# Optimization experiments

Hardware: AMD Instinct MI355X
Metric: run time of the kernel (lower is better)

Reference implementation:

```python
import jax, jax.numpy as jnp
import numpy as np

N = 100_000   # nodes
E = 1_600_000 # edges
F = 128       # feature_dim
H = 128       # hidden_dim
C = 16        # num_classes


def setup_inputs() -> dict:
    key = jax.random.key(0)
    ks = jax.random.split(key, 7)
    x = jax.random.normal(ks[0], (N, F), dtype=jnp.float32)
    edge_index = jax.random.randint(ks[1], (2, E), 0, N, dtype=jnp.int64)
    edge_attr = jax.random.uniform(ks[2], (E,), dtype=jnp.float32)
    W1 = jax.random.normal(ks[3], (F, H), dtype=jnp.float32) / np.float32(np.sqrt(F))
    b1 = jnp.zeros((H,), jnp.float32)
    W2 = jax.random.normal(ks[4], (H, C), dtype=jnp.float32) / np.float32(np.sqrt(H))
    b2 = jnp.zeros((C,), jnp.float32)
    return {"x": x, "edge_index": edge_index, "edge_attr": edge_attr,
            "W1": W1, "b1": b1, "W2": W2, "b2": b2}


def gcn_conv(x, src, dst, ew, W, b, n):
    # PyG GCNConv: add self-loops (weight 1), symmetric degree normalization,
    # linear transform, weighted scatter-sum to destinations, bias after aggregation.
    loop = jnp.arange(n, dtype=src.dtype)
    s = jnp.concatenate([src, loop])
    d = jnp.concatenate([dst, loop])
    w = jnp.concatenate([ew, jnp.ones((n,), ew.dtype)])
    deg = jax.ops.segment_sum(w, d, num_segments=n)           # [N]
    dinv = jnp.where(deg > 0, jax.lax.rsqrt(deg), 0.0)
    norm = dinv[s] * w * dinv[d]                               # [E+N]
    h = x @ W                                                  # [N, out]
    out = jax.ops.segment_sum(h[s] * norm[:, None], d, num_segments=n)
    return out + b


def reference(x, edge_index, edge_attr, W1, b1, W2, b2):
    src, dst = edge_index[0], edge_index[1]
    h = gcn_conv(x, src, dst, edge_attr, W1, b1, N)
    h = jax.nn.relu(h)
    # dropout is identity in eval mode
    h = gcn_conv(h, src, dst, edge_attr, W2, b2, N)
    return jax.nn.softmax(h, axis=1)
```

## Files before the change

kernel.cpp:

```cpp
#include <hip/hip_runtime.h>
#include <hip/hip_fp16.h>
#include <math.h>

#define SCAN_CHUNK 2048
#define NBLK 256
#define BSH 9
#define BNODES 512


typedef __attribute__((ext_vector_type(8))) _Float16 f16x8;
typedef __attribute__((ext_vector_type(16))) float f32x16;


__global__ __launch_bounds__(256) void k_prep(const float* __restrict__ W,
                                              __half* __restrict__ W1f) {
    int tid = blockIdx.x * 256 + threadIdx.x;
    if (tid < 16384) {
        int j  = tid & 7;
        int l  = (tid >> 3) & 63;
        int ks = (tid >> 9) & 7;
        int cb = tid >> 12;
        int c = cb * 32 + (l & 31);
        int k = (l >> 5) * 8 + ks * 16 + j;
        W1f[tid] = __float2half(W[(size_t)k * 128 + c]);
    }
}


__device__ __forceinline__ void gemm1_mfma(const float* __restrict__ x,
                                           const __half* __restrict__ W1f,
                                           __half* __restrict__ h1, int n,
                                           int row0, int t, char* smem) {
    __half (*xs)[136] = (__half (*)[136])smem;
#pragma unroll
    for (int it = 0; it < 4; ++it) {
        int idx = it * 256 + t;
        int r = idx >> 5, c4 = (idx & 31) * 4;
        int gr = row0 + r;
        float4 v = (gr < n) ? *(const float4*)(x + (size_t)gr * 128 + c4)
                            : make_float4(0.f, 0.f, 0.f, 0.f);
        union { __half2 h[2]; uint2 u; } pk;
        pk.h[0] = __floats2half2_rn(v.x, v.y);
        pk.h[1] = __floats2half2_rn(v.z, v.w);
        *(uint2*)&xs[r][c4] = pk.u;
    }
    __syncthreads();

    int wv = t >> 6, lane = t & 63;
    int m = lane & 31, kh = lane >> 5;
    int col0 = wv * 32;

    f16x8 a[8], b[8];
    const __half* bp = W1f + ((size_t)wv * 8 * 64 + lane) * 8;
#pragma unroll
    for (int ks = 0; ks < 8; ++ks)
        b[ks] = *(const f16x8*)(bp + (size_t)ks * 64 * 8);
#pragma unroll
    for (int ks = 0; ks < 8; ++ks)
        a[ks] = *(const f16x8*)&xs[m][kh * 8 + ks * 16];

    f32x16 acc;
#pragma unroll
    for (int r = 0; r < 16; ++r) acc[r] = 0.f;
#pragma unroll
    for (int ks = 0; ks < 8; ++ks)
        acc = __builtin_amdgcn_mfma_f32_32x32x16_f16(a[ks], b[ks], acc, 0, 0, 0);

#pragma unroll
    for (int r = 0; r < 16; ++r) {
        int row = (r & 3) + 8 * (r >> 2) + 4 * kh;
        int g = row0 + row;
        if (g < n) h1[(size_t)g * 128 + col0 + m] = __float2half(acc[r]);
    }
}

__device__ __forceinline__ long long sl_begin(int eb, int e) {
    return ((long long)eb * e / NBLK) & ~3LL;
}


__global__ __launch_bounds__(256) void kA(const int* __restrict__ dst, int e,
                                          int* __restrict__ hist, int nbuck,
                                          const float* __restrict__ x,
                                          const __half* __restrict__ W1f,
                                          __half* __restrict__ h1, int n,
                                          int nbB, int nbG, int gbase) {
    __shared__ char smem[32 * 136 * 2];
    int bid = blockIdx.x;
    long long T = nbB + nbG;
    long long g = ((long long)bid * nbG) / T;
    bool is_g = (((long long)(bid + 1) * nbG) / T) > g;
    int t = threadIdx.x;

    if (!is_g) {
        int* cnt = (int*)smem;
        int eb = bid - (int)g;
        for (int j = t; j < nbuck; j += 256) cnt[j] = 0;
        __syncthreads();
        long long e0 = sl_begin(eb, e);
        long long e1 = (eb == NBLK - 1) ? e : sl_begin(eb + 1, e);
        for (long long i = e0 + (long long)t * 4; i + 3 < e1; i += 1024) {
            int4 d4 = *(const int4*)(dst + i);
            atomicAdd(&cnt[d4.x >> BSH], 1);
            atomicAdd(&cnt[d4.y >> BSH], 1);
            atomicAdd(&cnt[d4.z >> BSH], 1);
            atomicAdd(&cnt[d4.w >> BSH], 1);
        }
        long long vend = e0 + ((e1 - e0) & ~3LL);
        for (long long i = vend + t; i < e1; i += 256)
            atomicAdd(&cnt[dst[i] >> BSH], 1);
        __syncthreads();
        for (int j = t; j < nbuck; j += 256)
            hist[(size_t)j * NBLK + eb] = cnt[j];
        return;
    }

    gemm1_mfma(x, W1f, h1, n, (gbase + (int)g) * 32, t, smem);
}


__global__ __launch_bounds__(256) void k_scanh(int* __restrict__ hist,
                                               int* __restrict__ bsum, int nh) {
    __shared__ int sh[256];
    int b = blockIdx.x, t = threadIdx.x;
    int base = b * SCAN_CHUNK + t * 8;
    int v[8];
    int s = 0;
#pragma unroll
    for (int j = 0; j < 8; ++j) {
        int i = base + j;
        v[j] = (i < nh) ? hist[i] : 0;
        s += v[j];
    }
    sh[t] = s;
    __syncthreads();
    for (int off = 1; off < 256; off <<= 1) {
        int u = (t >= off) ? sh[t - off] : 0;
        __syncthreads();
        sh[t] += u;
        __syncthreads();
    }
    int excl = (t > 0) ? sh[t - 1] : 0;
    if (t == 255) bsum[b] = sh[255];
    int run = excl;
#pragma unroll
    for (int j = 0; j < 8; ++j) {
        int i = base + j;
        if (i < nh) hist[i] = run;
        run += v[j];
    }
}

__device__ __forceinline__ void scan_bsum(const int* __restrict__ bsum, int nbS,
                                          int* boffs, int t) {
    if (t < 32) {
        int raw = (t < nbS) ? bsum[t] : 0;
        int v = raw;
        for (int off = 1; off < 32; off <<= 1) {
            int u = __shfl_up(v, off, 64);
            if (t >= off) v += u;
        }
        boffs[t] = v - raw;
    }
}


__global__ __launch_bounds__(256) void kB(const int* __restrict__ src,
                                          const int* __restrict__ dst,
                                          const float* __restrict__ ew, int e,
                                          const int* __restrict__ hist,
                                          const int* __restrict__ bsum, int nbS,
                                          int nbuck,
                                          int2* __restrict__ bucketed,
                                          const float* __restrict__ x,
                                          const __half* __restrict__ W1f,
                                          __half* __restrict__ h1, int n,
                                          int nbB, int nbG, int gbase) {
    __shared__ char smem[32 * 136 * 2];
    int bid = blockIdx.x;
    long long T = nbB + nbG;
    long long g = ((long long)bid * nbG) / T;
    bool is_g = (((long long)(bid + 1) * nbG) / T) > g;
    int t = threadIdx.x;

    if (!is_g) {
        int* wc = (int*)smem;
        int* boffs = (int*)(smem + 2048);
        int eb = bid - (int)g;
        scan_bsum(bsum, nbS, boffs, t);
        __syncthreads();
        for (int j = t; j < nbuck; j += 256) {
            int idx = j * NBLK + eb;
            wc[j] = hist[idx] + boffs[idx >> 11];
        }
        __syncthreads();
        long long e0 = sl_begin(eb, e);
        long long e1 = (eb == NBLK - 1) ? e : sl_begin(eb + 1, e);
        for (long long i = e0 + (long long)t * 4; i + 3 < e1; i += 1024) {
            int4 d4 = *(const int4*)(dst + i);
            int4 s4 = *(const int4*)(src + i);
            float4 w4 = *(const float4*)(ew + i);
            int2 rec;
            int pos;
            pos = atomicAdd(&wc[d4.x >> BSH], 1);
            rec.x = s4.x | ((d4.x & (BNODES - 1)) << 17);
            rec.y = __float_as_int(w4.x);
            bucketed[pos] = rec;
            pos = atomicAdd(&wc[d4.y >> BSH], 1);
            rec.x = s4.y | ((d4.y & (BNODES - 1)) << 17);
            rec.y = __float_as_int(w4.y);
            bucketed[pos] = rec;
            pos = atomicAdd(&wc[d4.z >> BSH], 1);
            rec.x = s4.z | ((d4.z & (BNODES - 1)) << 17);
            rec.y = __float_as_int(w4.z);
            bucketed[pos] = rec;
            pos = atomicAdd(&wc[d4.w >> BSH], 1);
            rec.x = s4.w | ((d4.w & (BNODES - 1)) << 17);
            rec.y = __float_as_int(w4.w);
            bucketed[pos] = rec;
        }
        long long vend = e0 + ((e1 - e0) & ~3LL);
        for (long long i = vend + t; i < e1; i += 256) {
            int d = dst[i];
            int b = d >> BSH;
            int pos = atomicAdd(&wc[b], 1);
            int2 rec;
            rec.x = src[i] | ((d & (BNODES - 1)) << 17);
            rec.y = __float_as_int(ew[i]);
            bucketed[pos] = rec;
        }
        return;
    }

    gemm1_mfma(x, W1f, h1, n, (gbase + (int)g) * 32, t, smem);
}


__global__ __launch_bounds__(256) void kC1(const int2* __restrict__ bucketed,
                                           const int* __restrict__ hist,
                                           const int* __restrict__ bsum, int nbS,
                                           int nbuck, int n, int e,
                                           int2* __restrict__ nodeinfo,
                                           const float* __restrict__ x,
                                           const __half* __restrict__ W1f,
                                           __half* __restrict__ h1, int gbase) {
    __shared__ char smem[32 * 136 * 2];
    int bid = blockIdx.x, t = threadIdx.x;

    if (bid >= nbuck) {
        gemm1_mfma(x, W1f, h1, n, (gbase + bid - nbuck) * 32, t, smem);
        return;
    }

    unsigned long long* cd = (unsigned long long*)smem;
    int* sh    = (int*)(smem + 4096);
    int* boffs = (int*)(smem + 5120);
    int b = bid;

    scan_bsum(bsum, nbS, boffs, t);
    cd[t] = 0ULL; cd[t + 256] = 0ULL;
    __syncthreads();

    int i0 = b * NBLK;
    int bstart = hist[i0] + boffs[i0 >> 11];
    int bend;
    if (b == nbuck - 1) bend = e;
    else {
        int i1 = (b + 1) * NBLK;
        bend = hist[i1] + boffs[i1 >> 11];
    }

    for (int i = bstart + t; i < bend; i += 256) {
        int2 rec = bucketed[i];
        int l = (rec.x >> 17) & (BNODES - 1);
        unsigned long long pk = (1ULL << 52) |
            (unsigned long long)(long long)rintf(__int_as_float(rec.y) * 67108864.0f);
        atomicAdd(&cd[l], pk);
    }
    __syncthreads();

    unsigned long long v0 = cd[2 * t], v1 = cd[2 * t + 1];
    int c0 = (int)(v0 >> 52), c1 = (int)(v1 >> 52);
    float d0 = (float)(long long)(v0 & ((1ULL << 52) - 1)) * 1.4901161193847656e-8f;
    float d1 = (float)(long long)(v1 & ((1ULL << 52) - 1)) * 1.4901161193847656e-8f;
    sh[t] = c0 + c1;
    __syncthreads();
    for (int off = 1; off < 256; off <<= 1) {
        int u = (t >= off) ? sh[t - off] : 0;
        __syncthreads();
        sh[t] += u;
        __syncthreads();
    }
    int excl = (t > 0) ? sh[t - 1] : 0;

    int rs0 = bstart + excl;
    int rs1 = rs0 + c0;
#pragma unroll
    for (int q = 0; q < 2; ++q) {
        int l = 2 * t + q;
        float dv = 1.0f / sqrtf(1.0f + ((q == 0) ? d0 : d1));
        int gnode = b * BNODES + l;
        if (gnode < n) {
            int2 ni;
            ni.x = (q == 0) ? rs0 : rs1;
            ni.y = __float_as_int(dv);
            nodeinfo[gnode] = ni;
        }
    }
    if (b == nbuck - 1 && t == 0) {
        int2 sent; sent.x = e; sent.y = 0;
        nodeinfo[n] = sent;
    }
}


__global__ __launch_bounds__(256) void kC2(const int2* __restrict__ bucketed,
                                           const int* __restrict__ hist,
                                           const int* __restrict__ bsum, int nbS,
                                           int nbuck, int n, int e,
                                           int2* __restrict__ csr,
                                           const int2* __restrict__ nodeinfo,
                                           const float* __restrict__ x,
                                           const __half* __restrict__ W1f,
                                           __half* __restrict__ h1, int gbase) {
    __shared__ char smem[32 * 136 * 2];
    int bid = blockIdx.x, t = threadIdx.x;

    if (bid >= nbuck) {
        gemm1_mfma(x, W1f, h1, n, (gbase + bid - nbuck) * 32, t, smem);
        return;
    }

    int* wcs   = (int*)smem;
    int* boffs = (int*)(smem + 2048);
    int b = bid;
    const int* nis = (const int*)nodeinfo;

    scan_bsum(bsum, nbS, boffs, t);
#pragma unroll
    for (int q = 0; q < 2; ++q) {
        int l = t + q * 256;
        int gnode = b * BNODES + l;
        wcs[l] = (gnode < n) ? nis[2 * (size_t)gnode] : 0;
    }
    __syncthreads();

    int i0 = b * NBLK;
    int bstart = hist[i0] + boffs[i0 >> 11];
    int bend;
    if (b == nbuck - 1) bend = e;
    else {
        int i1 = (b + 1) * NBLK;
        bend = hist[i1] + boffs[i1 >> 11];
    }

    for (int i = bstart + t; i < bend; i += 256) {
        int2 rec = bucketed[i];
        int l = (rec.x >> 17) & (BNODES - 1);
        int s = rec.x & 0x1FFFF;
        float dv = __int_as_float(nis[2 * (size_t)s + 1]);
        int pos = atomicAdd(&wcs[l], 1);
        int2 o;
        o.x = s;
        o.y = __float_as_int(__int_as_float(rec.y) * dv);
        csr[pos] = o;
    }
}


__global__ __launch_bounds__(256) void k_agg1(const __half* __restrict__ h1,
                                              const int2* __restrict__ nodeinfo,
                                              const int2* __restrict__ csr,
                                              const float* __restrict__ b1,
                                              const float* __restrict__ W2g,
                                              __half* __restrict__ h2, int n) {
    __shared__ float a1s[4][128];
    __shared__ float wt[16][132];
    int t = threadIdx.x;
#pragma unroll
    for (int it = 0; it < 8; ++it) {
        int idx = it * 256 + t;
        wt[idx & 15][idx >> 4] = W2g[idx];
    }
    int wv = t >> 6;
    int lane = t & 63;
    int grp = lane >> 4;
    int sl = lane & 15;
    int i = blockIdx.x * 4 + wv;
    float acc[8];
#pragma unroll
    for (int k = 0; k < 8; ++k) acc[k] = 0.f;
    float di = 0.f;
    if (i < n) {
        int2 ni = nodeinfo[i];
        int begin = ni.x;
        int end = ((const int*)nodeinfo)[(size_t)(i + 1) * 2];
        di = __int_as_float(ni.y);
        if (grp == 0) {
            uint4 sv = *((const uint4*)(h1 + (size_t)i * 128) + sl);
            const __half2* hp = (const __half2*)&sv;
#pragma unroll
            for (int k = 0; k < 4; ++k) {
                float2 f = __half22float2(hp[k]);
                acc[2 * k] = di * f.x; acc[2 * k + 1] = di * f.y;
            }
        }
        int len = end - begin;
        int m = (len + 3) >> 2;
        if (m > 0) {
            int j0 = begin + grp;
            bool v0 = j0 < end;
            int2 er0 = csr[v0 ? j0 : begin];
            float w0 = v0 ? __int_as_float(er0.y) : 0.f;
            uint4 hv0 = *((const uint4*)(h1 + (size_t)er0.x * 128) + sl);
            int j1 = j0 + 4;
            bool v1 = j1 < end;
            int2 er1 = csr[v1 ? j1 : begin];
            float w1 = v1 ? __int_as_float(er1.y) : 0.f;
            for (int it2 = 1; it2 < m; ++it2) {
                uint4 hv1 = *((const uint4*)(h1 + (size_t)er1.x * 128) + sl);
                int j2 = j1 + 4;
                bool v2 = j2 < end;
                int2 er2 = csr[v2 ? j2 : begin];
                float w2 = v2 ? __int_as_float(er2.y) : 0.f;
                const __half2* hp = (const __half2*)&hv0;
#pragma unroll
                for (int k = 0; k < 4; ++k) {
                    float2 f = __half22float2(hp[k]);
                    acc[2 * k]     += w0 * f.x;
                    acc[2 * k + 1] += w0 * f.y;
                }
                hv0 = hv1; w0 = w1;
                er1 = er2; w1 = w2; j1 = j2;
            }
            const __half2* hp = (const __half2*)&hv0;
#pragma unroll
            for (int k = 0; k < 4; ++k) {
                float2 f = __half22float2(hp[k]);
                acc[2 * k]     += w0 * f.x;
                acc[2 * k + 1] += w0 * f.y;
            }
        }
    }
#pragma unroll
    for (int k = 0; k < 8; ++k) {
        acc[k] += __shfl_xor(acc[k], 16, 64);
        acc[k] += __shfl_xor(acc[k], 32, 64);
    }
    if (i < n && grp == 0) {
#pragma unroll
        for (int k = 0; k < 8; ++k)
            a1s[wv][8 * sl + k] = fmaxf(di * acc[k] + b1[8 * sl + k], 0.f);
    }
    __syncthreads();
    int oi = t >> 2, q = t & 3;
    int node = oi >> 4, c = oi & 15;
    const float* arow = a1s[node];
    float accd = 0.f;
#pragma unroll
    for (int j = 0; j < 32; ++j) accd += arow[q + 4 * j] * wt[c][q + 4 * j];
    accd += __shfl_xor(accd, 1, 64);
    accd += __shfl_xor(accd, 2, 64);
    int gi = blockIdx.x * 4 + node;
    if (q == 0 && gi < n) h2[(size_t)gi * 16 + c] = __float2half(accd);
}


__global__ __launch_bounds__(256) void k_agg2(const __half* __restrict__ h2,
                                              const int2* __restrict__ nodeinfo,
                                              const int2* __restrict__ csr,
                                              const float* __restrict__ b2,
                                              float* __restrict__ out, int n) {
    int t = blockIdx.x * 256 + threadIdx.x;
    int i = t >> 3;
    int cp = t & 7;
    if (i >= n) return;
    int2 ni = nodeinfo[i];
    int begin = ni.x;
    int end = ((const int*)nodeinfo)[(size_t)(i + 1) * 2];
    float di = __int_as_float(ni.y);
    const __half2* h2p = (const __half2*)h2;
    float2 self = __half22float2(h2p[(size_t)i * 8 + cp]);
    float a0 = di * self.x, a1 = di * self.y;
    int j = begin;
    for (; j + 4 <= end; j += 4) {
        int2 e0 = csr[j], e1 = csr[j + 1], e2 = csr[j + 2], e3 = csr[j + 3];
        float2 f0 = __half22float2(h2p[(size_t)e0.x * 8 + cp]);
        float2 f1 = __half22float2(h2p[(size_t)e1.x * 8 + cp]);
        float2 f2 = __half22float2(h2p[(size_t)e2.x * 8 + cp]);
        float2 f3 = __half22float2(h2p[(size_t)e3.x * 8 + cp]);
        float w0 = __int_as_float(e0.y), w1 = __int_as_float(e1.y);
        float w2 = __int_as_float(e2.y), w3 = __int_as_float(e3.y);
        a0 += w0 * f0.x; a1 += w0 * f0.y;
        a0 += w1 * f1.x; a1 += w1 * f1.y;
        a0 += w2 * f2.x; a1 += w2 * f2.y;
        a0 += w3 * f3.x; a1 += w3 * f3.y;
    }
    for (; j < end; ++j) {
        int2 e0 = csr[j];
        float2 f0 = __half22float2(h2p[(size_t)e0.x * 8 + cp]);
        float w0 = __int_as_float(e0.y);
        a0 += w0 * f0.x; a1 += w0 * f0.y;
    }
    float2 bb = *(const float2*)(b2 + 2 * cp);
    a0 = di * a0 + bb.x;
    a1 = di * a1 + bb.y;
    float m = fmaxf(a0, a1);
    for (int off = 4; off; off >>= 1) m = fmaxf(m, __shfl_xor(m, off, 8));
    float ex0 = expf(a0 - m), ex1 = expf(a1 - m);
    float s = ex0 + ex1;
    for (int off = 4; off; off >>= 1) s += __shfl_xor(s, off, 8);
    float2 o; o.x = ex0 / s; o.y = ex1 / s;
    *(float2*)(out + (size_t)i * 16 + 2 * cp) = o;
}


extern "C" void kernel_launch(void* const* d_in, const int* in_sizes, int n_in,
                              void* d_out, int out_size, void* d_ws, size_t ws_size,
                              hipStream_t stream) {
    const float* x  = (const float*)d_in[0];
    const int*   ei = (const int*)d_in[1];
    const float* ew = (const float*)d_in[2];
    const float* W1 = (const float*)d_in[3];
    const float* b1 = (const float*)d_in[4];
    const float* W2 = (const float*)d_in[5];
    const float* b2 = (const float*)d_in[6];
    float* out = (float*)d_out;

    const int N = in_sizes[0] / 128;
    const int E = in_sizes[2];
    const int* src = ei;
    const int* dst = ei + E;

    const int nbuck = (N + BNODES - 1) >> BSH;
    const int nh = nbuck * NBLK;
    const int nbS = (nh + SCAN_CHUNK - 1) / SCAN_CHUNK;

    char* w = (char*)d_ws;
    int2*   bucketed = (int2*)w;              w += (size_t)E * 8;
    int2*   csr      = (int2*)w;              w += (size_t)E * 8;
    __half* h1       = (__half*)w;            w += (size_t)N * 128 * 2;
    __half* h2       = (__half*)w;            w += (size_t)N * 16 * 2;
    int2*   nodeinfo = (int2*)w;              w += (size_t)(N + 2) * 8;
    int*    hist     = (int*)w;               w += (size_t)nh * 4;
    int*    bsum     = (int*)w;               w += 64 * 4;
    __half* W1f      = (__half*)w;            w += (size_t)16384 * 2;

    int nbG_total = (N + 31) / 32;
    int nbG1 = 1450;
    int nbG2 = 1150;
    int nbG3 = 275;
    int nbG4 = nbG_total - nbG1 - nbG2 - nbG3;

    k_prep<<<64, 256, 0, stream>>>(W1, W1f);
    kA<<<NBLK + nbG1, 256, 0, stream>>>(dst, E, hist, nbuck, x, W1f, h1, N,
                                        NBLK, nbG1, 0);
    k_scanh<<<nbS, 256, 0, stream>>>(hist, bsum, nh);
    kB<<<NBLK + nbG2, 256, 0, stream>>>(src, dst, ew, E, hist, bsum, nbS, nbuck,
                                        bucketed, x, W1f, h1, N, NBLK, nbG2, nbG1);
    kC1<<<nbuck + nbG3, 256, 0, stream>>>(bucketed, hist, bsum, nbS, nbuck, N, E,
                                          nodeinfo, x, W1f, h1, nbG1 + nbG2);
    kC2<<<nbuck + nbG4, 256, 0, stream>>>(bucketed, hist, bsum, nbS, nbuck, N, E,
                                          csr, nodeinfo, x, W1f, h1,
                                          nbG1 + nbG2 + nbG3);
    k_agg1<<<(N + 3) / 4, 256, 0, stream>>>(h1, nodeinfo, csr, b1, W2, h2, N);
    k_agg2<<<(N + 31) / 32, 256, 0, stream>>>(h2, nodeinfo, csr, b2, out, N);
}
```

Measured before the change: 178.7 us.

## Process four GEMM row tiles per block with double-buffered LDS prefetch

```diff
diff --git a/kernel.cpp b/kernel.cpp
--- a/kernel.cpp
+++ b/kernel.cpp
@@ -6,10 +6,13 @@
 #define NBLK 256
 #define BSH 9
 #define BNODES 512
+#define NT 4
 
 
 typedef __attribute__((ext_vector_type(8))) _Float16 f16x8;
 typedef __attribute__((ext_vector_type(16))) float f32x16;
+
+#define GEMM_SMEM (64 * 136 * 2)
 
 
 __global__ __launch_bounds__(256) void k_prep(const float* __restrict__ W,
@@ -27,50 +30,87 @@
 }
 
 
-__device__ __forceinline__ void gemm1_mfma(const float* __restrict__ x,
-                                           const __half* __restrict__ W1f,
-                                           __half* __restrict__ h1, int n,
-                                           int row0, int t, char* smem) {
+__device__ __forceinline__ void gemm1_tiles(const float* __restrict__ x,
+                                            const __half* __restrict__ W1f,
+                                            __half* __restrict__ h1, int n,
+                                            int tile0, int t, char* smem) {
     __half (*xs)[136] = (__half (*)[136])smem;
-#pragma unroll
-    for (int it = 0; it < 4; ++it) {
-        int idx = it * 256 + t;
-        int r = idx >> 5, c4 = (idx & 31) * 4;
-        int gr = row0 + r;
-        float4 v = (gr < n) ? *(const float4*)(x + (size_t)gr * 128 + c4)
-                            : make_float4(0.f, 0.f, 0.f, 0.f);
-        union { __half2 h[2]; uint2 u; } pk;
-        pk.h[0] = __floats2half2_rn(v.x, v.y);
-        pk.h[1] = __floats2half2_rn(v.z, v.w);
-        *(uint2*)&xs[r][c4] = pk.u;
-    }
-    __syncthreads();
+    int ntt = (n + 31) >> 5;
+    int ntile = ntt - tile0;
+    if (ntile > NT) ntile = NT;
 
     int wv = t >> 6, lane = t & 63;
     int m = lane & 31, kh = lane >> 5;
     int col0 = wv * 32;
 
-    f16x8 a[8], b[8];
+    f16x8 b[8];
     const __half* bp = W1f + ((size_t)wv * 8 * 64 + lane) * 8;
 #pragma unroll
     for (int ks = 0; ks < 8; ++ks)
         b[ks] = *(const f16x8*)(bp + (size_t)ks * 64 * 8);
-#pragma unroll
-    for (int ks = 0; ks < 8; ++ks)
-        a[ks] = *(const f16x8*)&xs[m][kh * 8 + ks * 16];
-
-    f32x16 acc;
-#pragma unroll
-    for (int r = 0; r < 16; ++r) acc[r] = 0.f;
-#pragma unroll
-    for (int ks = 0; ks < 8; ++ks)
-        acc = __builtin_amdgcn_mfma_f32_32x32x16_f16(a[ks], b[ks], acc, 0, 0, 0);
-
-#pragma unroll
-    for (int r = 0; r < 16; ++r) {
-        int row = (r & 3) + 8 * (r >> 2) + 4 * kh;
-        int g = row0 + row;
-        if (g < n) h1[(size_t)g * 128 + col0 + m] = __float2half(acc[r]);
+
+    float4 v[4];
+    int row0 = tile0 * 32;
+#pragma unroll
+    for (int it = 0; it < 4; ++it) {
+        int idx = it * 256 + t;
+        int rr = idx >> 5, c4 = (idx & 31) * 4;
+        int gr = row0 + rr;
+        v[it] = (gr < n) ? *(const float4*)(x + (size_t)gr * 128 + c4)
+                         : make_float4(0.f, 0.f, 0.f, 0.f);
+    }
+    int cur = 0;
+#pragma unroll
+    for (int it = 0; it < 4; ++it) {
+        int idx = it * 256 + t;
+        int rr = idx >> 5, c4 = (idx & 31) * 4;
+        union { __half2 h[2]; uint2 u; } pk;
+        pk.h[0] = __floats2half2_rn(v[it].x, v[it].y);
+        pk.h[1] = __floats2half2_rn(v[it].z, v[it].w);
+        *(uint2*)&xs[rr][c4] = pk.u;
+    }
+    __syncthreads();
+
+    for (int tt = 0; tt < ntile; ++tt) {
+        int rowc = (tile0 + tt) * 32;
+        if (tt + 1 < ntile) {
+            int rown = rowc + 32;
+#pragma unroll
+            for (int it = 0; it < 4; ++it) {
+                int idx = it * 256 + t;
+                int rr = idx >> 5, c4 = (idx & 31) * 4;
+                int gr = rown + rr;
+                v[it] = (gr < n) ? *(const float4*)(x + (size_t)gr * 128 + c4)
+                                 : make_float4(0.f, 0.f, 0.f, 0.f);
+            }
+        }
+        f32x16 acc;
+#pragma unroll
+        for (int q = 0; q < 16; ++q) acc[q] = 0.f;
+#pragma unroll
+        for (int ks = 0; ks < 8; ++ks) {
+            f16x8 a = *(const f16x8*)&xs[cur * 32 + m][kh * 8 + ks * 16];
+            acc = __builtin_amdgcn_mfma_f32_32x32x16_f16(a, b[ks], acc, 0, 0, 0);
+        }
+#pragma unroll
+        for (int q = 0; q < 16; ++q) {
+            int row = (q & 3) + 8 * (q >> 2) + 4 * kh;
+            int g = rowc + row;
+            if (g < n) h1[(size_t)g * 128 + col0 + m] = __float2half(acc[q]);
+        }
+        if (tt + 1 < ntile) {
+#pragma unroll
+            for (int it = 0; it < 4; ++it) {
+                int idx = it * 256 + t;
+                int rr = idx >> 5, c4 = (idx & 31) * 4;
+                union { __half2 h[2]; uint2 u; } pk;
+                pk.h[0] = __floats2half2_rn(v[it].x, v[it].y);
+                pk.h[1] = __floats2half2_rn(v[it].z, v[it].w);
+                *(uint2*)&xs[(cur ^ 1) * 32 + rr][c4] = pk.u;
+            }
+            __syncthreads();
+            cur ^= 1;
+        }
     }
 }
 
@@ -85,7 +125,7 @@
                                           const __half* __restrict__ W1f,
                                           __half* __restrict__ h1, int n,
                                           int nbB, int nbG, int gbase) {
-    __shared__ char smem[32 * 136 * 2];
+    __shared__ char smem[GEMM_SMEM];
     int bid = blockIdx.x;
     long long T = nbB + nbG;
     long long g = ((long long)bid * nbG) / T;
@@ -115,7 +155,7 @@
         return;
     }
 
-    gemm1_mfma(x, W1f, h1, n, (gbase + (int)g) * 32, t, smem);
+    gemm1_tiles(x, W1f, h1, n, (gbase + (int)g) * NT, t, smem);
 }
 
 
@@ -176,7 +216,7 @@
                                           const __half* __restrict__ W1f,
                                           __half* __restrict__ h1, int n,
                                           int nbB, int nbG, int gbase) {
-    __shared__ char smem[32 * 136 * 2];
+    __shared__ char smem[GEMM_SMEM];
     int bid = blockIdx.x;
     long long T = nbB + nbG;
     long long g = ((long long)bid * nbG) / T;
@@ -232,7 +272,7 @@
         return;
     }
 
-    gemm1_mfma(x, W1f, h1, n, (gbase + (int)g) * 32, t, smem);
+    gemm1_tiles(x, W1f, h1, n, (gbase + (int)g) * NT, t, smem);
 }
 
 
@@ -244,11 +284,11 @@
                                            const float* __restrict__ x,
                                            const __half* __restrict__ W1f,
                                            __half* __restrict__ h1, int gbase) {
-    __shared__ char smem[32 * 136 * 2];
+    __shared__ char smem[GEMM_SMEM];
     int bid = blockIdx.x, t = threadIdx.x;
 
     if (bid >= nbuck) {
-        gemm1_mfma(x, W1f, h1, n, (gbase + bid - nbuck) * 32, t, smem);
+        gemm1_tiles(x, W1f, h1, n, (gbase + bid - nbuck) * NT, t, smem);
         return;
     }
 
@@ -323,11 +363,11 @@
                                            const float* __restrict__ x,
                                            const __half* __restrict__ W1f,
                                            __half* __restrict__ h1, int gbase) {
-    __shared__ char smem[32 * 136 * 2];
+    __shared__ char smem[GEMM_SMEM];
     int bid = blockIdx.x, t = threadIdx.x;
 
     if (bid >= nbuck) {
-        gemm1_mfma(x, W1f, h1, n, (gbase + bid - nbuck) * 32, t, smem);
+        gemm1_tiles(x, W1f, h1, n, (gbase + bid - nbuck) * NT, t, smem);
         return;
     }
 
@@ -546,23 +586,24 @@
     int*    bsum     = (int*)w;               w += 64 * 4;
     __half* W1f      = (__half*)w;            w += (size_t)16384 * 2;
 
-    int nbG_total = (N + 31) / 32;
-    int nbG1 = 1450;
-    int nbG2 = 1150;
-    int nbG3 = 275;
-    int nbG4 = nbG_total - nbG1 - nbG2 - nbG3;
+    int ntiles = (N + 31) / 32;
+    int tbTotal = (ntiles + NT - 1) / NT;
+    int tbA = 360;
+    int tbB = 290;
+    int tbC1 = 70;
+    int tbC2 = tbTotal - tbA - tbB - tbC1;
 
     k_prep<<<64, 256, 0, stream>>>(W1, W1f);
-    kA<<<NBLK + nbG1, 256, 0, stream>>>(dst, E, hist, nbuck, x, W1f, h1, N,
-                                        NBLK, nbG1, 0);
+    kA<<<NBLK + tbA, 256, 0, stream>>>(dst, E, hist, nbuck, x, W1f, h1, N,
+                                       NBLK, tbA, 0);
     k_scanh<<<nbS, 256, 0, stream>>>(hist, bsum, nh);
-    kB<<<NBLK + nbG2, 256, 0, stream>>>(src, dst, ew, E, hist, bsum, nbS, nbuck,
-                                        bucketed, x, W1f, h1, N, NBLK, nbG2, nbG1);
-    kC1<<<nbuck + nbG3, 256, 0, stream>>>(bucketed, hist, bsum, nbS, nbuck, N, E,
-                                          nodeinfo, x, W1f, h1, nbG1 + nbG2);
-    kC2<<<nbuck + nbG4, 256, 0, stream>>>(bucketed, hist, bsum, nbS, nbuck, N, E,
+    kB<<<NBLK + tbB, 256, 0, stream>>>(src, dst, ew, E, hist, bsum, nbS, nbuck,
+                                       bucketed, x, W1f, h1, N, NBLK, tbB, tbA);
+    kC1<<<nbuck + tbC1, 256, 0, stream>>>(bucketed, hist, bsum, nbS, nbuck, N, E,
+                                          nodeinfo, x, W1f, h1, tbA + tbB);
+    kC2<<<nbuck + tbC2, 256, 0, stream>>>(bucketed, hist, bsum, nbS, nbuck, N, E,
                                           csr, nodeinfo, x, W1f, h1,
-                                          nbG1 + nbG2 + nbG3);
+                                          tbA + tbB + tbC1);
     k_agg1<<<(N + 3) / 4, 256, 0, stream>>>(h1, nodeinfo, csr, b1, W2, h2, N);
     k_agg2<<<(N + 31) / 32, 256, 0, stream>>>(h2, nodeinfo, csr, b2, out, N);
 }
```

Measured after the change: 180.4 us. No clear change (+0.9%).

## Merge CSR build and GEMM1 into one cooperative persistent kernel

Applied to the files above, without the earlier changes.

```diff
diff --git a/kernel.cpp b/kernel.cpp
--- a/kernel.cpp
+++ b/kernel.cpp
@@ -1,11 +1,14 @@
 #include <hip/hip_runtime.h>
 #include <hip/hip_fp16.h>
+#include <hip/hip_cooperative_groups.h>
 #include <math.h>
 
-#define SCAN_CHUNK 2048
+namespace cg = cooperative_groups;
+
 #define NBLK 256
 #define BSH 9
 #define BNODES 512
+#define CG_GRID 512
 
 
 typedef __attribute__((ext_vector_type(8))) _Float16 f16x8;
@@ -13,7 +16,10 @@
 
 
 __global__ __launch_bounds__(256) void k_prep(const float* __restrict__ W,
-                                              __half* __restrict__ W1f) {
+                                              __half* __restrict__ W1f,
+                                              int* __restrict__ tot,
+                                              int* __restrict__ gcur,
+                                              int* __restrict__ ctrs) {
     int tid = blockIdx.x * 256 + threadIdx.x;
     if (tid < 16384) {
         int j  = tid & 7;
@@ -24,14 +30,20 @@
         int k = (l >> 5) * 8 + ks * 16 + j;
         W1f[tid] = __float2half(W[(size_t)k * 128 + c]);
     }
-}
-
-
-__device__ __forceinline__ void gemm1_mfma(const float* __restrict__ x,
-                                           const __half* __restrict__ W1f,
-                                           __half* __restrict__ h1, int n,
-                                           int row0, int t, char* smem) {
+    if (tid < 256) { tot[tid] = 0; gcur[tid] = 0; }
+    if (tid < 8) ctrs[tid] = 0;
+}
+
+__device__ __forceinline__ long long sl_begin(int eb, int e) {
+    return ((long long)eb * e / NBLK) & ~3LL;
+}
+
+__device__ __forceinline__ void do_gemm(const float* __restrict__ x,
+                                        const f16x8 b[8],
+                                        __half* __restrict__ h1, int n,
+                                        int tile, int t, char* smem) {
     __half (*xs)[136] = (__half (*)[136])smem;
+    int row0 = tile * 32;
 #pragma unroll
     for (int it = 0; it < 4; ++it) {
         int idx = it * 256 + t;
@@ -45,58 +57,64 @@
         *(uint2*)&xs[r][c4] = pk.u;
     }
     __syncthreads();
-
     int wv = t >> 6, lane = t & 63;
     int m = lane & 31, kh = lane >> 5;
     int col0 = wv * 32;
-
-    f16x8 a[8], b[8];
-    const __half* bp = W1f + ((size_t)wv * 8 * 64 + lane) * 8;
-#pragma unroll
-    for (int ks = 0; ks < 8; ++ks)
-        b[ks] = *(const f16x8*)(bp + (size_t)ks * 64 * 8);
-#pragma unroll
-    for (int ks = 0; ks < 8; ++ks)
-        a[ks] = *(const f16x8*)&xs[m][kh * 8 + ks * 16];
-
     f32x16 acc;
 #pragma unroll
-    for (int r = 0; r < 16; ++r) acc[r] = 0.f;
-#pragma unroll
-    for (int ks = 0; ks < 8; ++ks)
-        acc = __builtin_amdgcn_mfma_f32_32x32x16_f16(a[ks], b[ks], acc, 0, 0, 0);
-
-#pragma unroll
-    for (int r = 0; r < 16; ++r) {
-        int row = (r & 3) + 8 * (r >> 2) + 4 * kh;
+    for (int q = 0; q < 16; ++q) acc[q] = 0.f;
+#pragma unroll
+    for (int ks = 0; ks < 8; ++ks) {
+        f16x8 a = *(const f16x8*)&xs[m][kh * 8 + ks * 16];
+        acc = __builtin_amdgcn_mfma_f32_32x32x16_f16(a, b[ks], acc, 0, 0, 0);
+    }
+#pragma unroll
+    for (int q = 0; q < 16; ++q) {
+        int row = (q & 3) + 8 * (q >> 2) + 4 * kh;
         int g = row0 + row;
-        if (g < n) h1[(size_t)g * 128 + col0 + m] = __float2half(acc[r]);
-    }
-}
-
-__device__ __forceinline__ long long sl_begin(int eb, int e) {
-    return ((long long)eb * e / NBLK) & ~3LL;
-}
-
-
-__global__ __launch_bounds__(256) void kA(const int* __restrict__ dst, int e,
-                                          int* __restrict__ hist, int nbuck,
-                                          const float* __restrict__ x,
-                                          const __half* __restrict__ W1f,
-                                          __half* __restrict__ h1, int n,
-                                          int nbB, int nbG, int gbase) {
-    __shared__ char smem[32 * 136 * 2];
-    int bid = blockIdx.x;
-    long long T = nbB + nbG;
-    long long g = ((long long)bid * nbG) / T;
-    bool is_g = (((long long)(bid + 1) * nbG) / T) > g;
-    int t = threadIdx.x;
-
-    if (!is_g) {
+        if (g < n) h1[(size_t)g * 128 + col0 + m] = __float2half(acc[q]);
+    }
+}
+
+__device__ __forceinline__ int pull(int* ctr, int lo, int hi, int t, int* sP) {
+    if (t == 0) *sP = lo + atomicAdd(ctr, 1);
+    __syncthreads();
+    int v = *sP;
+    return (v < hi) ? v : -1;
+}
+
+
+__global__ __launch_bounds__(256, 4) void k_coop(
+        const int* __restrict__ src, const int* __restrict__ dst,
+        const float* __restrict__ ew, int e, int nbuck, int n,
+        const float* __restrict__ x, const __half* __restrict__ W1f,
+        __half* __restrict__ h1,
+        int2* __restrict__ bucketed, int2* __restrict__ csr,
+        int2* __restrict__ nodeinfo,
+        int* __restrict__ tot, int* __restrict__ gcur,
+        int* __restrict__ gbase, int* __restrict__ ctrs,
+        int ntiles, int cap1, int cap2, int cap3) {
+    __shared__ char smem[8704];
+    __shared__ int sPull;
+    cg::grid_group grid = cg::this_grid();
+    int bid = blockIdx.x, t = threadIdx.x;
+
+    int wv = t >> 6, lane = t & 63;
+    f16x8 b[8];
+    {
+        const __half* bp = W1f + ((size_t)wv * 8 * 64 + lane) * 8;
+#pragma unroll
+        for (int ks = 0; ks < 8; ++ks)
+            b[ks] = *(const f16x8*)(bp + (size_t)ks * 64 * 8);
+    }
+
+    int c0r = 0, c1r = 0;
+
+    if (bid < NBLK) {
         int* cnt = (int*)smem;
-        int eb = bid - (int)g;
-        for (int j = t; j < nbuck; j += 256) cnt[j] = 0;
-        __syncthreads();
+        cnt[t] = 0; cnt[t + 256] = 0;
+        __syncthreads();
+        int eb = bid;
         long long e0 = sl_begin(eb, e);
         long long e1 = (eb == NBLK - 1) ? e : sl_begin(eb + 1, e);
         for (long long i = e0 + (long long)t * 4; i + 3 < e1; i += 1024) {
@@ -110,90 +128,37 @@
         for (long long i = vend + t; i < e1; i += 256)
             atomicAdd(&cnt[dst[i] >> BSH], 1);
         __syncthreads();
-        for (int j = t; j < nbuck; j += 256)
-            hist[(size_t)j * NBLK + eb] = cnt[j];
-        return;
-    }
-
-    gemm1_mfma(x, W1f, h1, n, (gbase + (int)g) * 32, t, smem);
-}
-
-
-__global__ __launch_bounds__(256) void k_scanh(int* __restrict__ hist,
-                                               int* __restrict__ bsum, int nh) {
-    __shared__ int sh[256];
-    int b = blockIdx.x, t = threadIdx.x;
-    int base = b * SCAN_CHUNK + t * 8;
-    int v[8];
-    int s = 0;
-#pragma unroll
-    for (int j = 0; j < 8; ++j) {
-        int i = base + j;
-        v[j] = (i < nh) ? hist[i] : 0;
-        s += v[j];
-    }
-    sh[t] = s;
-    __syncthreads();
-    for (int off = 1; off < 256; off <<= 1) {
-        int u = (t >= off) ? sh[t - off] : 0;
-        __syncthreads();
-        sh[t] += u;
-        __syncthreads();
-    }
-    int excl = (t > 0) ? sh[t - 1] : 0;
-    if (t == 255) bsum[b] = sh[255];
-    int run = excl;
-#pragma unroll
-    for (int j = 0; j < 8; ++j) {
-        int i = base + j;
-        if (i < nh) hist[i] = run;
-        run += v[j];
-    }
-}
-
-__device__ __forceinline__ void scan_bsum(const int* __restrict__ bsum, int nbS,
-                                          int* boffs, int t) {
-    if (t < 32) {
-        int raw = (t < nbS) ? bsum[t] : 0;
-        int v = raw;
-        for (int off = 1; off < 32; off <<= 1) {
-            int u = __shfl_up(v, off, 64);
-            if (t >= off) v += u;
-        }
-        boffs[t] = v - raw;
-    }
-}
-
-
-__global__ __launch_bounds__(256) void kB(const int* __restrict__ src,
-                                          const int* __restrict__ dst,
-                                          const float* __restrict__ ew, int e,
-                                          const int* __restrict__ hist,
-                                          const int* __restrict__ bsum, int nbS,
-                                          int nbuck,
-                                          int2* __restrict__ bucketed,
-                                          const float* __restrict__ x,
-                                          const __half* __restrict__ W1f,
-                                          __half* __restrict__ h1, int n,
-                                          int nbB, int nbG, int gbase) {
-    __shared__ char smem[32 * 136 * 2];
-    int bid = blockIdx.x;
-    long long T = nbB + nbG;
-    long long g = ((long long)bid * nbG) / T;
-    bool is_g = (((long long)(bid + 1) * nbG) / T) > g;
-    int t = threadIdx.x;
-
-    if (!is_g) {
+        c0r = cnt[2 * t]; c1r = cnt[2 * t + 1];
+        if (2 * t < nbuck && c0r) atomicAdd(&tot[2 * t], c0r);
+        if (2 * t + 1 < nbuck && c1r) atomicAdd(&tot[2 * t + 1], c1r);
+    }
+    for (int tl; (tl = pull(&ctrs[0], 0, cap1, t, &sPull)) >= 0; )
+        do_gemm(x, b, h1, n, tl, t, smem);
+    grid.sync();
+
+    if (bid < NBLK) {
         int* wc = (int*)smem;
-        int* boffs = (int*)(smem + 2048);
-        int eb = bid - (int)g;
-        scan_bsum(bsum, nbS, boffs, t);
-        __syncthreads();
-        for (int j = t; j < nbuck; j += 256) {
-            int idx = j * NBLK + eb;
-            wc[j] = hist[idx] + boffs[idx >> 11];
-        }
-        __syncthreads();
+        int* bb = (int*)(smem + 1024);
+        int tv = (t < nbuck) ? tot[t] : 0;
+        bb[t] = tv;
+        __syncthreads();
+        for (int off = 1; off < 256; off <<= 1) {
+            int u = (t >= off) ? bb[t - off] : 0;
+            __syncthreads();
+            bb[t] += u;
+            __syncthreads();
+        }
+        int ex = bb[t] - tv;
+        if (bid == 0) gbase[t] = ex;
+        __syncthreads();
+        bb[t] = ex;
+        __syncthreads();
+        if (2 * t < nbuck)
+            wc[2 * t] = bb[2 * t] + atomicAdd(&gcur[2 * t], c0r);
+        if (2 * t + 1 < nbuck)
+            wc[2 * t + 1] = bb[2 * t + 1] + atomicAdd(&gcur[2 * t + 1], c1r);
+        __syncthreads();
+        int eb = bid;
         long long e0 = sl_begin(eb, e);
         long long e1 = (eb == NBLK - 1) ? e : sl_begin(eb + 1, e);
         for (long long i = e0 + (long long)t * 4; i + 3 < e1; i += 1024) {
@@ -222,149 +187,94 @@
         long long vend = e0 + ((e1 - e0) & ~3LL);
         for (long long i = vend + t; i < e1; i += 256) {
             int d = dst[i];
-            int b = d >> BSH;
-            int pos = atomicAdd(&wc[b], 1);
+            int pos = atomicAdd(&wc[d >> BSH], 1);
             int2 rec;
             rec.x = src[i] | ((d & (BNODES - 1)) << 17);
             rec.y = __float_as_int(ew[i]);
             bucketed[pos] = rec;
         }
-        return;
-    }
-
-    gemm1_mfma(x, W1f, h1, n, (gbase + (int)g) * 32, t, smem);
-}
-
-
-__global__ __launch_bounds__(256) void kC1(const int2* __restrict__ bucketed,
-                                           const int* __restrict__ hist,
-                                           const int* __restrict__ bsum, int nbS,
-                                           int nbuck, int n, int e,
-                                           int2* __restrict__ nodeinfo,
-                                           const float* __restrict__ x,
-                                           const __half* __restrict__ W1f,
-                                           __half* __restrict__ h1, int gbase) {
-    __shared__ char smem[32 * 136 * 2];
-    int bid = blockIdx.x, t = threadIdx.x;
-
-    if (bid >= nbuck) {
-        gemm1_mfma(x, W1f, h1, n, (gbase + bid - nbuck) * 32, t, smem);
-        return;
-    }
-
-    unsigned long long* cd = (unsigned long long*)smem;
-    int* sh    = (int*)(smem + 4096);
-    int* boffs = (int*)(smem + 5120);
-    int b = bid;
-
-    scan_bsum(bsum, nbS, boffs, t);
-    cd[t] = 0ULL; cd[t + 256] = 0ULL;
-    __syncthreads();
-
-    int i0 = b * NBLK;
-    int bstart = hist[i0] + boffs[i0 >> 11];
-    int bend;
-    if (b == nbuck - 1) bend = e;
-    else {
-        int i1 = (b + 1) * NBLK;
-        bend = hist[i1] + boffs[i1 >> 11];
-    }
-
-    for (int i = bstart + t; i < bend; i += 256) {
-        int2 rec = bucketed[i];
-        int l = (rec.x >> 17) & (BNODES - 1);
-        unsigned long long pk = (1ULL << 52) |
-            (unsigned long long)(long long)rintf(__int_as_float(rec.y) * 67108864.0f);
-        atomicAdd(&cd[l], pk);
-    }
-    __syncthreads();
-
-    unsigned long long v0 = cd[2 * t], v1 = cd[2 * t + 1];
-    int c0 = (int)(v0 >> 52), c1 = (int)(v1 >> 52);
-    float d0 = (float)(long long)(v0 & ((1ULL << 52) - 1)) * 1.4901161193847656e-8f;
-    float d1 = (float)(long long)(v1 & ((1ULL << 52) - 1)) * 1.4901161193847656e-8f;
-    sh[t] = c0 + c1;
-    __syncthreads();
-    for (int off = 1; off < 256; off <<= 1) {
-        int u = (t >= off) ? sh[t - off] : 0;
-        __syncthreads();
-        sh[t] += u;
-        __syncthreads();
-    }
-    int excl = (t > 0) ? sh[t - 1] : 0;
-
-    int rs0 = bstart + excl;
-    int rs1 = rs0 + c0;
-#pragma unroll
-    for (int q = 0; q < 2; ++q) {
-        int l = 2 * t + q;
-        float dv = 1.0f / sqrtf(1.0f + ((q == 0) ? d0 : d1));
-        int gnode = b * BNODES + l;
-        if (gnode < n) {
-            int2 ni;
-            ni.x = (q == 0) ? rs0 : rs1;
-            ni.y = __float_as_int(dv);
-            nodeinfo[gnode] = ni;
-        }
-    }
-    if (b == nbuck - 1 && t == 0) {
-        int2 sent; sent.x = e; sent.y = 0;
-        nodeinfo[n] = sent;
-    }
-}
-
-
-__global__ __launch_bounds__(256) void kC2(const int2* __restrict__ bucketed,
-                                           const int* __restrict__ hist,
-                                           const int* __restrict__ bsum, int nbS,
-                                           int nbuck, int n, int e,
-                                           int2* __restrict__ csr,
-                                           const int2* __restrict__ nodeinfo,
-                                           const float* __restrict__ x,
-                                           const __half* __restrict__ W1f,
-                                           __half* __restrict__ h1, int gbase) {
-    __shared__ char smem[32 * 136 * 2];
-    int bid = blockIdx.x, t = threadIdx.x;
-
-    if (bid >= nbuck) {
-        gemm1_mfma(x, W1f, h1, n, (gbase + bid - nbuck) * 32, t, smem);
-        return;
-    }
-
-    int* wcs   = (int*)smem;
-    int* boffs = (int*)(smem + 2048);
-    int b = bid;
-    const int* nis = (const int*)nodeinfo;
-
-    scan_bsum(bsum, nbS, boffs, t);
-#pragma unroll
-    for (int q = 0; q < 2; ++q) {
-        int l = t + q * 256;
-        int gnode = b * BNODES + l;
-        wcs[l] = (gnode < n) ? nis[2 * (size_t)gnode] : 0;
-    }
-    __syncthreads();
-
-    int i0 = b * NBLK;
-    int bstart = hist[i0] + boffs[i0 >> 11];
-    int bend;
-    if (b == nbuck - 1) bend = e;
-    else {
-        int i1 = (b + 1) * NBLK;
-        bend = hist[i1] + boffs[i1 >> 11];
-    }
-
-    for (int i = bstart + t; i < bend; i += 256) {
-        int2 rec = bucketed[i];
-        int l = (rec.x >> 17) & (BNODES - 1);
-        int s = rec.x & 0x1FFFF;
-        float dv = __int_as_float(nis[2 * (size_t)s + 1]);
-        int pos = atomicAdd(&wcs[l], 1);
-        int2 o;
-        o.x = s;
-        o.y = __float_as_int(__int_as_float(rec.y) * dv);
-        csr[pos] = o;
-    }
+    }
+    for (int tl; (tl = pull(&ctrs[1], cap1, cap2, t, &sPull)) >= 0; )
+        do_gemm(x, b, h1, n, tl, t, smem);
+    grid.sync();
+
+    if (bid < nbuck) {
+        unsigned long long* cd = (unsigned long long*)smem;
+        int* sh = (int*)(smem + 4096);
+        cd[t] = 0ULL; cd[t + 256] = 0ULL;
+        __syncthreads();
+        int bstart = gbase[bid];
+        int bend = (bid == nbuck - 1) ? e : gbase[bid + 1];
+        for (int i = bstart + t; i < bend; i += 256) {
+            int2 rec = bucketed[i];
+            int l = (rec.x >> 17) & (BNODES - 1);
+            unsigned long long pk = (1ULL << 52) |
+                (unsigned long long)(long long)rintf(__int_as_float(rec.y) * 67108864.0f);
+            atomicAdd(&cd[l], pk);
+        }
+        __syncthreads();
+        unsigned long long v0 = cd[2 * t], v1 = cd[2 * t + 1];
+        int cc0 = (int)(v0 >> 52), cc1 = (int)(v1 >> 52);
+        float dd0 = (float)(long long)(v0 & ((1ULL << 52) - 1)) * 1.4901161193847656e-8f;
+        float dd1 = (float)(long long)(v1 & ((1ULL << 52) - 1)) * 1.4901161193847656e-8f;
+        sh[t] = cc0 + cc1;
+        __syncthreads();
+        for (int off = 1; off < 256; off <<= 1) {
+            int u = (t >= off) ? sh[t - off] : 0;
+            __syncthreads();
+            sh[t] += u;
+            __syncthreads();
+        }
+        int excl = (t > 0) ? sh[t - 1] : 0;
+        int rs0 = bstart + excl;
+        int rs1 = rs0 + cc0;
+#pragma unroll
+        for (int q = 0; q < 2; ++q) {
+            int l = 2 * t + q;
+            float dv = 1.0f / sqrtf(1.0f + ((q == 0) ? dd0 : dd1));
+            int gnode = bid * BNODES + l;
+            if (gnode < n) {
+                int2 ni;
+                ni.x = (q == 0) ? rs0 : rs1;
+                ni.y = __float_as_int(dv);
+                nodeinfo[gnode] = ni;
+            }
+        }
+        if (bid == nbuck - 1 && t == 0) {
+            int2 sent; sent.x = e; sent.y = 0;
+            nodeinfo[n] = sent;
+        }
+    }
+    for (int tl; (tl = pull(&ctrs[2], cap2, cap3, t, &sPull)) >= 0; )
+        do_gemm(x, b, h1, n, tl, t, smem);
+    grid.sync();
+
+    if (bid < nbuck) {
+        int* wcs = (int*)smem;
+        const int* nis = (const int*)nodeinfo;
+#pragma unroll
+        for (int q = 0; q < 2; ++q) {
+            int l = t + q * 256;
+            int gnode = bid * BNODES + l;
+            wcs[l] = (gnode < n) ? nis[2 * (size_t)gnode] : 0;
+        }
+        __syncthreads();
+        int bstart = gbase[bid];
+        int bend = (bid == nbuck - 1) ? e : gbase[bid + 1];
+        for (int i = bstart + t; i < bend; i += 256) {
+            int2 rec = bucketed[i];
+            int l = (rec.x >> 17) & (BNODES - 1);
+            int s = rec.x & 0x1FFFF;
+            float dv = __int_as_float(nis[2 * (size_t)s + 1]);
+            int pos = atomicAdd(&wcs[l], 1);
+            int2 o;
+            o.x = s;
+            o.y = __float_as_int(__int_as_float(rec.y) * dv);
+            csr[pos] = o;
+        }
+    }
+    for (int tl; (tl = pull(&ctrs[3], cap3, ntiles, t, &sPull)) >= 0; )
+        do_gemm(x, b, h1, n, tl, t, smem);
 }
 
 
@@ -527,14 +437,12 @@
     const float* b2 = (const float*)d_in[6];
     float* out = (float*)d_out;
 
-    const int N = in_sizes[0] / 128;
-    const int E = in_sizes[2];
+    int N = in_sizes[0] / 128;
+    int E = in_sizes[2];
     const int* src = ei;
     const int* dst = ei + E;
 
-    const int nbuck = (N + BNODES - 1) >> BSH;
-    const int nh = nbuck * NBLK;
-    const int nbS = (nh + SCAN_CHUNK - 1) / SCAN_CHUNK;
+    int nbuck = (N + BNODES - 1) >> BSH;
 
     char* w = (char*)d_ws;
     int2*   bucketed = (int2*)w;              w += (size_t)E * 8;
@@ -542,27 +450,28 @@
     __half* h1       = (__half*)w;            w += (size_t)N * 128 * 2;
     __half* h2       = (__half*)w;            w += (size_t)N * 16 * 2;
     int2*   nodeinfo = (int2*)w;              w += (size_t)(N + 2) * 8;
-    int*    hist     = (int*)w;               w += (size_t)nh * 4;
-    int*    bsum     = (int*)w;               w += 64 * 4;
     __half* W1f      = (__half*)w;            w += (size_t)16384 * 2;
-
-    int nbG_total = (N + 31) / 32;
-    int nbG1 = 1450;
-    int nbG2 = 1150;
-    int nbG3 = 275;
-    int nbG4 = nbG_total - nbG1 - nbG2 - nbG3;
-
-    k_prep<<<64, 256, 0, stream>>>(W1, W1f);
-    kA<<<NBLK + nbG1, 256, 0, stream>>>(dst, E, hist, nbuck, x, W1f, h1, N,
-                                        NBLK, nbG1, 0);
-    k_scanh<<<nbS, 256, 0, stream>>>(hist, bsum, nh);
-    kB<<<NBLK + nbG2, 256, 0, stream>>>(src, dst, ew, E, hist, bsum, nbS, nbuck,
-                                        bucketed, x, W1f, h1, N, NBLK, nbG2, nbG1);
-    kC1<<<nbuck + nbG3, 256, 0, stream>>>(bucketed, hist, bsum, nbS, nbuck, N, E,
-                                          nodeinfo, x, W1f, h1, nbG1 + nbG2);
-    kC2<<<nbuck + nbG4, 256, 0, stream>>>(bucketed, hist, bsum, nbS, nbuck, N, E,
-                                          csr, nodeinfo, x, W1f, h1,
-                                          nbG1 + nbG2 + nbG3);
+    int*    tot      = (int*)w;               w += 256 * 4;
+    int*    gcur     = (int*)w;               w += 256 * 4;
+    int*    gbase    = (int*)w;               w += 256 * 4;
+    int*    ctrs     = (int*)w;               w += 16 * 4;
+
+    int ntiles = (N + 31) / 32;
+    int cap1 = ntiles / 6;
+    int cap2 = ntiles / 2;
+    int cap3 = (ntiles * 3) / 4;
+
+    k_prep<<<64, 256, 0, stream>>>(W1, W1f, tot, gcur, ctrs);
+
+    void* cargs[] = { (void*)&src, (void*)&dst, (void*)&ew, (void*)&E,
+                      (void*)&nbuck, (void*)&N,
+                      (void*)&x, (void*)&W1f, (void*)&h1,
+                      (void*)&bucketed, (void*)&csr, (void*)&nodeinfo,
+                      (void*)&tot, (void*)&gcur, (void*)&gbase, (void*)&ctrs,
+                      (void*)&ntiles, (void*)&cap1, (void*)&cap2, (void*)&cap3 };
+    hipLaunchCooperativeKernel((void*)k_coop, dim3(CG_GRID), dim3(256),
+                               cargs, 0, stream);
+
     k_agg1<<<(N + 3) / 4, 256, 0, stream>>>(h1, nodeinfo, csr, b1, W2, h2, N);
     k_agg2<<<(N + 31) / 32, 256, 0, stream>>>(h2, nodeinfo, csr, b2, out, N);
 }
```

Result: slower. 389.1 us (+117.7%).

## Stage bucket scatter and CSR fill through shared memory for coalesced writes

Applied to the files above, without the earlier changes.

```diff
diff --git a/kernel.cpp b/kernel.cpp
--- a/kernel.cpp
+++ b/kernel.cpp
@@ -6,6 +6,8 @@
 #define NBLK 256
 #define BSH 9
 #define BNODES 512
+#define KB_CH 2048
+#define C2CAP 4608
 
 
 typedef __attribute__((ext_vector_type(8))) _Float16 f16x8;
@@ -85,7 +87,7 @@
                                           const __half* __restrict__ W1f,
                                           __half* __restrict__ h1, int n,
                                           int nbB, int nbG, int gbase) {
-    __shared__ char smem[32 * 136 * 2];
+    __shared__ char smem[8704];
     int bid = blockIdx.x;
     long long T = nbB + nbG;
     long long g = ((long long)bid * nbG) / T;
@@ -176,7 +178,7 @@
                                           const __half* __restrict__ W1f,
                                           __half* __restrict__ h1, int n,
                                           int nbB, int nbG, int gbase) {
-    __shared__ char smem[32 * 136 * 2];
+    __shared__ char smem[24704];
     int bid = blockIdx.x;
     long long T = nbB + nbG;
     long long g = ((long long)bid * nbG) / T;
@@ -184,8 +186,13 @@
     int t = threadIdx.x;
 
     if (!is_g) {
-        int* wc = (int*)smem;
-        int* boffs = (int*)(smem + 2048);
+        int2*  sbuf = (int2*)smem;
+        short* sbk  = (short*)(smem + 16384);
+        int*   wc   = (int*)(smem + 20480);
+        int*   lcnt = (int*)(smem + 21504);
+        int*   lst  = (int*)(smem + 22528);
+        int*   ssc  = (int*)(smem + 23552);
+        int*   boffs= (int*)(smem + 24576);
         int eb = bid - (int)g;
         scan_bsum(bsum, nbS, boffs, t);
         __syncthreads();
@@ -196,38 +203,54 @@
         __syncthreads();
         long long e0 = sl_begin(eb, e);
         long long e1 = (eb == NBLK - 1) ? e : sl_begin(eb + 1, e);
-        for (long long i = e0 + (long long)t * 4; i + 3 < e1; i += 1024) {
-            int4 d4 = *(const int4*)(dst + i);
-            int4 s4 = *(const int4*)(src + i);
-            float4 w4 = *(const float4*)(ew + i);
-            int2 rec;
-            int pos;
-            pos = atomicAdd(&wc[d4.x >> BSH], 1);
-            rec.x = s4.x | ((d4.x & (BNODES - 1)) << 17);
-            rec.y = __float_as_int(w4.x);
-            bucketed[pos] = rec;
-            pos = atomicAdd(&wc[d4.y >> BSH], 1);
-            rec.x = s4.y | ((d4.y & (BNODES - 1)) << 17);
-            rec.y = __float_as_int(w4.y);
-            bucketed[pos] = rec;
-            pos = atomicAdd(&wc[d4.z >> BSH], 1);
-            rec.x = s4.z | ((d4.z & (BNODES - 1)) << 17);
-            rec.y = __float_as_int(w4.z);
-            bucketed[pos] = rec;
-            pos = atomicAdd(&wc[d4.w >> BSH], 1);
-            rec.x = s4.w | ((d4.w & (BNODES - 1)) << 17);
-            rec.y = __float_as_int(w4.w);
-            bucketed[pos] = rec;
-        }
-        long long vend = e0 + ((e1 - e0) & ~3LL);
-        for (long long i = vend + t; i < e1; i += 256) {
-            int d = dst[i];
-            int b = d >> BSH;
-            int pos = atomicAdd(&wc[b], 1);
-            int2 rec;
-            rec.x = src[i] | ((d & (BNODES - 1)) << 17);
-            rec.y = __float_as_int(ew[i]);
-            bucketed[pos] = rec;
+        for (long long c0 = e0; c0 < e1; c0 += KB_CH) {
+            long long rem = e1 - c0;
+            int cn = (rem < (long long)KB_CH) ? (int)rem : KB_CH;
+            lcnt[t] = 0;
+            __syncthreads();
+            int myb[8], myr[8];
+#pragma unroll
+            for (int k = 0; k < 8; ++k) {
+                int i = t + k * 256;
+                if (i < cn) {
+                    int bck = dst[c0 + i] >> BSH;
+                    myb[k] = bck;
+                    myr[k] = atomicAdd(&lcnt[bck], 1);
+                } else myb[k] = -1;
+            }
+            __syncthreads();
+            int v = lcnt[t];
+            ssc[t] = v;
+            __syncthreads();
+            for (int off = 1; off < 256; off <<= 1) {
+                int u = (t >= off) ? ssc[t - off] : 0;
+                __syncthreads();
+                ssc[t] += u;
+                __syncthreads();
+            }
+            lst[t] = ssc[t] - v;
+            __syncthreads();
+#pragma unroll
+            for (int k = 0; k < 8; ++k) {
+                if (myb[k] >= 0) {
+                    long long i = c0 + t + k * 256;
+                    int d = dst[i];
+                    int2 rec;
+                    rec.x = src[i] | ((d & (BNODES - 1)) << 17);
+                    rec.y = __float_as_int(ew[i]);
+                    int slot = lst[myb[k]] + myr[k];
+                    sbuf[slot] = rec;
+                    sbk[slot] = (short)myb[k];
+                }
+            }
+            __syncthreads();
+            for (int i = t; i < cn; i += 256) {
+                int bck = sbk[i];
+                bucketed[wc[bck] + (i - lst[bck])] = sbuf[i];
+            }
+            __syncthreads();
+            if (t < nbuck) wc[t] += lcnt[t];
+            __syncthreads();
         }
         return;
     }
@@ -244,7 +267,7 @@
                                            const float* __restrict__ x,
                                            const __half* __restrict__ W1f,
                                            __half* __restrict__ h1, int gbase) {
-    __shared__ char smem[32 * 136 * 2];
+    __shared__ char smem[8704];
     int bid = blockIdx.x, t = threadIdx.x;
 
     if (bid >= nbuck) {
@@ -323,7 +346,7 @@
                                            const float* __restrict__ x,
                                            const __half* __restrict__ W1f,
                                            __half* __restrict__ h1, int gbase) {
-    __shared__ char smem[32 * 136 * 2];
+    __shared__ char smem[C2CAP * 8 + 2048 + 128];
     int bid = blockIdx.x, t = threadIdx.x;
 
     if (bid >= nbuck) {
@@ -331,39 +354,68 @@
         return;
     }
 
-    int* wcs   = (int*)smem;
-    int* boffs = (int*)(smem + 2048);
-    int b = bid;
+    int2* sbuf = (int2*)smem;
+    int* wcs   = (int*)(smem + C2CAP * 8);
+    int* boffs = (int*)(smem + C2CAP * 8 + 2048);
     const int* nis = (const int*)nodeinfo;
 
     scan_bsum(bsum, nbS, boffs, t);
+    __syncthreads();
+    int i0 = bid * NBLK;
+    int bstart = hist[i0] + boffs[i0 >> 11];
+    int bend;
+    if (bid == nbuck - 1) bend = e;
+    else {
+        int i1 = (bid + 1) * NBLK;
+        bend = hist[i1] + boffs[i1 >> 11];
+    }
+
 #pragma unroll
     for (int q = 0; q < 2; ++q) {
         int l = t + q * 256;
-        int gnode = b * BNODES + l;
-        wcs[l] = (gnode < n) ? nis[2 * (size_t)gnode] : 0;
-    }
-    __syncthreads();
-
-    int i0 = b * NBLK;
-    int bstart = hist[i0] + boffs[i0 >> 11];
-    int bend;
-    if (b == nbuck - 1) bend = e;
-    else {
-        int i1 = (b + 1) * NBLK;
-        bend = hist[i1] + boffs[i1 >> 11];
-    }
-
-    for (int i = bstart + t; i < bend; i += 256) {
-        int2 rec = bucketed[i];
-        int l = (rec.x >> 17) & (BNODES - 1);
-        int s = rec.x & 0x1FFFF;
-        float dv = __int_as_float(nis[2 * (size_t)s + 1]);
-        int pos = atomicAdd(&wcs[l], 1);
-        int2 o;
-        o.x = s;
-        o.y = __float_as_int(__int_as_float(rec.y) * dv);
-        csr[pos] = o;
+        int gnode = bid * BNODES + l;
+        wcs[l] = (gnode < n) ? nis[2 * (size_t)gnode] : e;
+    }
+    __syncthreads();
+    int r0 = wcs[0];
+    int r1 = wcs[256];
+    int r2 = bend;
+
+    for (int pass = 0; pass < 2; ++pass) {
+        int rlo = pass ? r1 : r0;
+        int rhi = pass ? r2 : r1;
+        int sz = rhi - rlo;
+        if (sz <= C2CAP) {
+            for (int i = bstart + t; i < bend; i += 256) {
+                int2 rec = bucketed[i];
+                int l = (rec.x >> 17) & (BNODES - 1);
+                if ((l >> 8) != pass) continue;
+                int s = rec.x & 0x1FFFF;
+                float dv = __int_as_float(nis[2 * (size_t)s + 1]);
+                int pos = atomicAdd(&wcs[l], 1);
+                int2 o;
+                o.x = s;
+                o.y = __float_as_int(__int_as_float(rec.y) * dv);
+                sbuf[pos - rlo] = o;
+            }
+            __syncthreads();
+            for (int i = t; i < sz; i += 256) csr[rlo + i] = sbuf[i];
+            __syncthreads();
+        } else {
+            for (int i = bstart + t; i < bend; i += 256) {
+                int2 rec = bucketed[i];
+                int l = (rec.x >> 17) & (BNODES - 1);
+                if ((l >> 8) != pass) continue;
+                int s = rec.x & 0x1FFFF;
+                float dv = __int_as_float(nis[2 * (size_t)s + 1]);
+                int pos = atomicAdd(&wcs[l], 1);
+                int2 o;
+                o.x = s;
+                o.y = __float_as_int(__int_as_float(rec.y) * dv);
+                csr[pos] = o;
+            }
+            __syncthreads();
+        }
     }
 }
 
```

Result: slower. 198.1 us (+10.8%).
